# Kernel optimization log

Hardware: AMD Instinct MI355X
Metric: run time of the kernel (lower is better)

The kernel has to match this reference:

```python
import jax, jax.numpy as jnp
import numpy as np

D_MODEL = 768
N_LAYER = 2
VOCAB = 32000
D_STATE = 16
D_INNER = 1536
DT_RANK = 48
D_CONV = 4
B, L = 2, 1024
EPS = 1e-5


def rmsnorm(x, w):
    return x * jax.lax.rsqrt(jnp.mean(x * x, axis=-1, keepdims=True) + EPS) * w


def selective_scan(u, dt, A, Bm, Cm, Dv):
    # u: (b,l,d)  dt: (b,l,d)  A: (d,n)  Bm,Cm: (b,l,n)  Dv: (d,)
    dA = jnp.einsum('bld,dn->bldn', dt, A)
    dB_u = jnp.einsum('bld,bld,bln->bldn', dt, u, Bm)
    # shift dA left by one step along l, zero-pad at end, reverse-cumsum, exp
    t = jnp.concatenate([dA[:, 1:], jnp.zeros_like(dA[:, :1])], axis=1)
    dA_cumsum = jnp.exp(jnp.flip(jnp.cumsum(jnp.flip(t, axis=1), axis=1), axis=1))
    x = dB_u * dA_cumsum
    x = jnp.cumsum(x, axis=1) / (dA_cumsum + 1e-12)
    y = jnp.einsum('bldn,bln->bld', x, Cm)
    return y + u * Dv


def mamba_block(x, W_in, conv_w, conv_b, x_proj_w, dt_proj_w, dt_proj_b, A_log, D_param, W_out):
    b, l, d = x.shape
    xz = x @ W_in.T                       # (b,l,2*d_inner)
    xs, res = xz[..., :D_INNER], xz[..., D_INNER:]
    # depthwise causal conv1d: left-pad d_conv-1 -> output length l
    xt = jnp.transpose(xs, (0, 2, 1))     # (b,d_in,l)
    xt = jax.lax.conv_general_dilated(
        xt, conv_w, window_strides=(1,), padding=[(D_CONV - 1, 0)],
        dimension_numbers=('NCH', 'OIH', 'NCH'), feature_group_count=D_INNER)
    xt = xt + conv_b[None, :, None]
    xs = jax.nn.silu(jnp.transpose(xt, (0, 2, 1)))
    # SSM
    A = -jnp.exp(A_log.astype(jnp.float32))
    x_dbl = xs @ x_proj_w.T               # (b,l,dt_rank+2n)
    delta = x_dbl[..., :DT_RANK]
    Bm = x_dbl[..., DT_RANK:DT_RANK + D_STATE]
    Cm = x_dbl[..., DT_RANK + D_STATE:]
    delta = jax.nn.softplus(delta @ dt_proj_w.T + dt_proj_b)
    y = selective_scan(xs, delta, A, Bm, Cm, D_param.astype(jnp.float32))
    y = y * jax.nn.silu(res)
    return y @ W_out.T


def setup_inputs() -> dict:
    key = jax.random.key(0)
    ks = jax.random.split(key, 12)
    s = 0.02
    inp = {
        'input_ids': jax.random.randint(ks[0], (B, L), 0, VOCAB),
        'embedding': jax.random.normal(ks[1], (VOCAB, D_MODEL), jnp.float32) * s,
        'W_in': jax.random.normal(ks[2], (N_LAYER, 2 * D_INNER, D_MODEL), jnp.float32) * s,
        'conv_w': jax.random.normal(ks[3], (N_LAYER, D_INNER, 1, D_CONV), jnp.float32) * 0.2,
        'conv_b': jnp.zeros((N_LAYER, D_INNER), jnp.float32),
        'x_proj_w': jax.random.normal(ks[4], (N_LAYER, DT_RANK + 2 * D_STATE, D_INNER), jnp.float32) * s,
        'dt_proj_w': jax.random.normal(ks[5], (N_LAYER, D_INNER, DT_RANK), jnp.float32) * s,
        'dt_proj_b': jnp.full((N_LAYER, D_INNER), -4.0, jnp.float32),
        'A_log': jnp.broadcast_to(jnp.log(jnp.arange(1, D_STATE + 1, dtype=jnp.float32)), (N_LAYER, D_INNER, D_STATE)) * jnp.ones((N_LAYER, D_INNER, 1), jnp.float32),
        'D_param': jnp.ones((N_LAYER, D_INNER), jnp.float32),
        'W_out': jax.random.normal(ks[6], (N_LAYER, D_MODEL, D_INNER), jnp.float32) * s,
        'norm_w': jnp.ones((N_LAYER, D_MODEL), jnp.float32),
        'norm_f_w': jnp.ones((D_MODEL,), jnp.float32),
    }
    return inp


def reference(input_ids, embedding, W_in, conv_w, conv_b, x_proj_w, dt_proj_w,
              dt_proj_b, A_log, D_param, W_out, norm_w, norm_f_w):
    x = embedding[input_ids]              # (b,l,d_model)
    for i in range(N_LAYER):
        x = mamba_block(rmsnorm(x, norm_w[i]), W_in[i], conv_w[i], conv_b[i],
                        x_proj_w[i], dt_proj_w[i], dt_proj_b[i], A_log[i],
                        D_param[i], W_out[i]) + x
    x = rmsnorm(x, norm_f_w)
    return x @ embedding.T                # tied lm_head -> (b,l,vocab)
```

## Files before the change

kernel.cpp:

```cpp
#include <hip/hip_runtime.h>
#include <math.h>

#define DM    768
#define DS    16
#define DI    1536
#define DTR   48
#define NB    2
#define NL    1024
#define NBL   (NB*NL)
#define NVOC  32000
#define XDL   128

typedef __attribute__((ext_vector_type(8))) short bf16x8;
typedef __attribute__((ext_vector_type(4))) float floatx4;

static __device__ __forceinline__ float siluf(float x){ return x / (1.0f + expf(-x)); }
static __device__ __forceinline__ float softplusf(float x){ return (x > 20.0f) ? x : log1pf(expf(x)); }
static __device__ __forceinline__ unsigned short f2bf(float f){
    unsigned int u = __float_as_uint(f);
    u += 0x7FFFu + ((u >> 16) & 1u);
    return (unsigned short)(u >> 16);
}

#define GLL16(g, l) __builtin_amdgcn_global_load_lds( \
    (const __attribute__((address_space(1))) unsigned int*)(g), \
    (__attribute__((address_space(3))) unsigned int*)(l), 16, 0, 0)

__global__ __launch_bounds__(256) void cast_bf16_kernel(const float* __restrict__ in,
        unsigned short* __restrict__ out, int n4){
    int i = blockIdx.x*256 + threadIdx.x;
    if (i >= n4) return;
    float4 v = ((const float4*)in)[i];
    ushort4 o = { f2bf(v.x), f2bf(v.y), f2bf(v.z), f2bf(v.w) };
    ((ushort4*)out)[i] = o;
}

__global__ __launch_bounds__(256) void cast_pad_xproj_kernel(const float* __restrict__ in,
        unsigned short* __restrict__ out){
    int q = blockIdx.x*256 + threadIdx.x;
    const int QL = 128*1536/4;
    if (q >= 2*QL) return;
    int layer = q / QL, rem = q - layer*QL;
    int row = rem / (1536/4), c4 = rem - row*(1536/4);
    ushort4 o = {0,0,0,0};
    if (row < 80){
        float4 v = ((const float4*)(in + ((size_t)layer*80 + row)*1536))[c4];
        o.x = f2bf(v.x); o.y = f2bf(v.y); o.z = f2bf(v.z); o.w = f2bf(v.w);
    }
    ((ushort4*)out)[q] = o;
}

__global__ __launch_bounds__(256) void zero_f32_kernel(float* __restrict__ p, int n4){
    int i = blockIdx.x*256 + threadIdx.x;
    if (i >= n4) return;
    float4 z = {0.f,0.f,0.f,0.f};
    ((float4*)p)[i] = z;
}

__global__ __launch_bounds__(256) void embed_kernel(const int* __restrict__ ids,
        const float* __restrict__ emb, float* __restrict__ x){
    int i = blockIdx.x*256 + threadIdx.x;
    if (i >= NBL*DM) return;
    int row = i / DM, c = i - row*DM;
    x[i] = emb[(size_t)ids[row]*DM + c];
}

__global__ __launch_bounds__(256) void rmsnorm_bf16_kernel(const float* __restrict__ x,
        const float* __restrict__ w, unsigned short* __restrict__ h){
    int row = blockIdx.x;
    const float* xr = x + (size_t)row*DM;
    __shared__ float red[256];
    float s = 0.f;
    for (int c = threadIdx.x; c < DM; c += 256){ float v = xr[c]; s += v*v; }
    red[threadIdx.x] = s; __syncthreads();
    for (int o = 128; o > 0; o >>= 1){
        if (threadIdx.x < o) red[threadIdx.x] += red[threadIdx.x + o];
        __syncthreads();
    }
    float r = 1.0f / sqrtf(red[0]*(1.0f/DM) + 1e-5f);
    for (int c = threadIdx.x; c < DM; c += 256) h[(size_t)row*DM + c] = f2bf(xr[c]*r*w[c]);
}

template<int MODE>
__global__ __launch_bounds__(256) void mfma_gemm_nt(const unsigned short* __restrict__ A,
        const unsigned short* __restrict__ B, float* __restrict__ C,
        int M, int N, int K, int Kc){
    __shared__ __align__(16) unsigned short Asm[128*32];
    __shared__ __align__(16) unsigned short Bsm[128*32];
    int tid = threadIdx.x;

    int nwg  = gridDim.x * gridDim.y;
    int orig = blockIdx.y * gridDim.x + blockIdx.x;
    int q = nwg >> 3, r = nwg & 7;
    int xcd = orig & 7;
    int wg  = (xcd < r ? xcd*(q+1) : r*(q+1) + (xcd-r)*q) + (orig >> 3);
    int mb  = wg % gridDim.y;
    int nb  = wg / gridDim.y;
    int m0 = mb * 128, n0 = nb * 128;

    int lane = tid & 63;
    int quad = lane >> 4, l16 = lane & 15;
    int wave = tid >> 6;
    int wm = (wave >> 1) * 64, wn = (wave & 1) * 64;

    floatx4 acc[4][4] = {};

    int srow = tid >> 2, skcol = (tid & 3) * 8;
    const unsigned short* Ag = A + (size_t)(m0 + srow) * K + skcol;
    const unsigned short* Bg = B + (size_t)(n0 + srow) * K + skcol;
    size_t half = (size_t)64 * K;

    int k0 = blockIdx.z * Kc;
    for (int kt = k0; kt < k0 + Kc; kt += 32){
        GLL16(Ag + kt,        &Asm[(size_t)tid*8]);
        GLL16(Ag + kt + half, &Asm[2048 + (size_t)tid*8]);
        GLL16(Bg + kt,        &Bsm[(size_t)tid*8]);
        GLL16(Bg + kt + half, &Bsm[2048 + (size_t)tid*8]);
        __syncthreads();

        bf16x8 af[4], bff[4];
        #pragma unroll
        for (int i = 0; i < 4; i++){
            af[i]  = *(const bf16x8*)&Asm[(wm + i*16 + l16)*32 + quad*8];
            bff[i] = *(const bf16x8*)&Bsm[(wn + i*16 + l16)*32 + quad*8];
        }
        #pragma unroll
        for (int i = 0; i < 4; i++)
            #pragma unroll
            for (int j = 0; j < 4; j++)
                acc[i][j] = __builtin_amdgcn_mfma_f32_16x16x32_bf16(af[i], bff[j], acc[i][j], 0, 0, 0);
        __syncthreads();
    }

    #pragma unroll
    for (int i = 0; i < 4; i++){
        int gm = m0 + wm + i*16 + quad*4;
        #pragma unroll
        for (int j = 0; j < 4; j++){
            int gn = n0 + wn + j*16 + l16;
            float* cp = C + (size_t)gm*N + gn;
            #pragma unroll
            for (int r = 0; r < 4; r++){
                float v = acc[i][j][r];
                if (MODE == 2){
                    atomicAdd(&cp[(size_t)r*N], v);
                } else {
                    if (MODE == 1) v += cp[(size_t)r*N];
                    cp[(size_t)r*N] = v;
                }
            }
        }
    }
}

__global__ __launch_bounds__(256) void gemm_nt(const float* __restrict__ A,
        const float* __restrict__ Bw, float* __restrict__ C, const float* __restrict__ bias,
        int M, int N, int K, int lda, int ldb, int ldc, int act, int accum){
    __shared__ float As[16][68];
    __shared__ float Bs[16][68];
    int tid = threadIdx.x;
    int tn = tid & 15, tm = tid >> 4;
    int n0 = blockIdx.x * 64, m0 = blockIdx.y * 64;
    float acc[4][4] = {{0.f}};
    for (int kt = 0; kt < K; kt += 16){
        int gk = kt + tn;
        bool kok = gk < K;
        #pragma unroll
        for (int r = 0; r < 4; r++){
            int m = tm + r*16;
            As[tn][m] = (kok && (m0 + m) < M) ? A[(size_t)(m0+m)*lda + gk] : 0.f;
            Bs[tn][m] = (kok && (n0 + m) < N) ? Bw[(size_t)(n0+m)*ldb + gk] : 0.f;
        }
        __syncthreads();
        #pragma unroll
        for (int kk = 0; kk < 16; kk++){
            float a0 = As[kk][tm*4+0], a1 = As[kk][tm*4+1], a2 = As[kk][tm*4+2], a3 = As[kk][tm*4+3];
            float b0 = Bs[kk][tn*4+0], b1 = Bs[kk][tn*4+1], b2 = Bs[kk][tn*4+2], b3 = Bs[kk][tn*4+3];
            acc[0][0] += a0*b0; acc[0][1] += a0*b1; acc[0][2] += a0*b2; acc[0][3] += a0*b3;
            acc[1][0] += a1*b0; acc[1][1] += a1*b1; acc[1][2] += a1*b2; acc[1][3] += a1*b3;
            acc[2][0] += a2*b0; acc[2][1] += a2*b1; acc[2][2] += a2*b2; acc[2][3] += a2*b3;
            acc[3][0] += a3*b0; acc[3][1] += a3*b1; acc[3][2] += a3*b2; acc[3][3] += a3*b3;
        }
        __syncthreads();
    }
    #pragma unroll
    for (int i = 0; i < 4; i++){
        int gm = m0 + tm*4 + i;
        if (gm >= M) continue;
        #pragma unroll
        for (int j = 0; j < 4; j++){
            int gn = n0 + tn*4 + j;
            if (gn >= N) continue;
            float v = acc[i][j];
            if (bias) v += bias[gn];
            if (act == 1) v = softplusf(v);
            size_t ci = (size_t)gm*ldc + gn;
            if (accum) v += C[ci];
            C[ci] = v;
        }
    }
}

__global__ __launch_bounds__(256) void conv_silu_kernel(const float* __restrict__ xz,
        const float* __restrict__ cw, const float* __restrict__ cb,
        float* __restrict__ xs, unsigned short* __restrict__ xs_bf){
    int i = blockIdx.x*256 + threadIdx.x;
    if (i >= NBL*DI) return;
    int bl = i / DI, d = i - bl*DI;
    int l = bl & (NL-1);
    float acc = cb[d];
    #pragma unroll
    for (int j = 0; j < 4; j++){
        int off = j - 3;
        if (l + off >= 0) acc += cw[d*4+j] * xz[(size_t)(bl + off)*(2*DI) + d];
    }
    float v = siluf(acc);
    xs[i] = v;
    xs_bf[i] = f2bf(v);
}

__global__ __launch_bounds__(256) void transpose_kernel(const float* __restrict__ in,
        float* __restrict__ out, int R, int Ccols, int ldin){
    __shared__ float tile[32][33];
    int c0 = blockIdx.x*32, r0 = blockIdx.y*32;
    int tx = threadIdx.x & 31, ty = threadIdx.x >> 5;
    #pragma unroll
    for (int i = 0; i < 32; i += 8){
        int r = r0 + ty + i, c = c0 + tx;
        tile[ty+i][tx] = (r < R && c < Ccols) ? in[(size_t)r*ldin + c] : 0.f;
    }
    __syncthreads();
    #pragma unroll
    for (int i = 0; i < 32; i += 8){
        int r = r0 + tx, c = c0 + ty + i;
        if (c < Ccols && r < R) out[(size_t)c*R + r] = tile[tx][ty+i];
    }
}

static __device__ __forceinline__ float block_scan_excl(float v, float* sbuf, float* total){
    int tid  = threadIdx.x;
    int lane = tid & 63, w = tid >> 6;
    float run = v;
    #pragma unroll
    for (int s = 1; s < 64; s <<= 1){
        float t = __shfl_up(run, s, 64);
        if (lane >= s) run += t;
    }
    if (lane == 63) sbuf[w] = run;
    __syncthreads();
    float w0 = sbuf[0], w1 = sbuf[1], w2 = sbuf[2], w3 = sbuf[3];
    __syncthreads();
    float wpre = 0.f;
    if (w > 0) wpre += w0;
    if (w > 1) wpre += w1;
    if (w > 2) wpre += w2;
    *total = w0 + w1 + w2 + w3;
    return wpre + run - v;
}

__global__ __launch_bounds__(256) void scan_kernel(const float* __restrict__ u_t,
        const float* dt_t, const float* __restrict__ xdbl_t,
        const float* __restrict__ A_log, const float* __restrict__ Dp,
        float* y_t){
    __shared__ float sbuf[8];
    int tid = threadIdx.x;
    int bd = blockIdx.x;
    int b = bd / DI, d = bd - b*DI;
    size_t rowoff = (size_t)d*NBL + b*NL;
    int l0 = tid*4;

    float4 dtv = *(const float4*)(dt_t + rowoff + l0);
    float4 uv  = *(const float4*)(u_t  + rowoff + l0);
    float d4[4] = {dtv.x, dtv.y, dtv.z, dtv.w};
    float u4[4] = {uv.x,  uv.y,  uv.z,  uv.w};
    float pl[4], du[4], yac[4] = {0.f,0.f,0.f,0.f};
    float run = 0.f;
    #pragma unroll
    for (int r = 0; r < 4; r++){ run += d4[r]; pl[r] = run; du[r] = d4[r]*u4[r]; }
    float T;
    float ex = block_scan_excl(run, sbuf, &T);
    #pragma unroll
    for (int r = 0; r < 4; r++) pl[r] += ex;

    for (int n = 0; n < DS; n++){
        float An = -expf(A_log[d*DS + n]);
        float4 Bv4 = *(const float4*)(xdbl_t + (size_t)(DTR+n)*NBL + b*NL + l0);
        float4 Cv4 = *(const float4*)(xdbl_t + (size_t)(DTR+DS+n)*NBL + b*NL + l0);
        float Bv[4] = {Bv4.x, Bv4.y, Bv4.z, Bv4.w};
        float Cv[4] = {Cv4.x, Cv4.y, Cv4.z, Cv4.w};
        float e[4], zl[4];
        float zrun = 0.f;
        #pragma unroll
        for (int r = 0; r < 4; r++){
            e[r] = expf(An * (T - pl[r]));
            zrun += du[r]*Bv[r]*e[r];
            zl[r] = zrun;
        }
        float zt;
        float zex = block_scan_excl(zrun, sbuf, &zt);
        #pragma unroll
        for (int r = 0; r < 4; r++){
            float num = zex + zl[r];
            float xv  = num / (e[r] + 1e-12f);
            yac[r] += xv * Cv[r];
        }
    }
    float Dv = Dp[d];
    float4 yo;
    yo.x = yac[0] + u4[0]*Dv;
    yo.y = yac[1] + u4[1]*Dv;
    yo.z = yac[2] + u4[2]*Dv;
    yo.w = yac[3] + u4[3]*Dv;
    *(float4*)(y_t + rowoff + l0) = yo;
}

__global__ __launch_bounds__(256) void gate_transpose_kernel(const float* __restrict__ y_t,
        const float* __restrict__ xz, unsigned short* __restrict__ ys){
    __shared__ float tile[32][33];
    int c0 = blockIdx.x*32;
    int r0 = blockIdx.y*32;
    int tx = threadIdx.x & 31, ty = threadIdx.x >> 5;
    #pragma unroll
    for (int i = 0; i < 32; i += 8)
        tile[ty+i][tx] = y_t[(size_t)(r0+ty+i)*NBL + (c0+tx)];
    __syncthreads();
    #pragma unroll
    for (int i = 0; i < 32; i += 8){
        int d  = r0 + tx;
        int bl = c0 + ty + i;
        float g = siluf(xz[(size_t)bl*(2*DI) + DI + d]);
        ys[(size_t)bl*DI + d] = f2bf(tile[tx][ty+i] * g);
    }
}

extern "C" void kernel_launch(void* const* d_in, const int* in_sizes, int n_in,
                              void* d_out, int out_size, void* d_ws, size_t ws_size,
                              hipStream_t stream){
    const int*   ids    = (const int*)d_in[0];
    const float* emb    = (const float*)d_in[1];
    const float* W_in   = (const float*)d_in[2];
    const float* convw  = (const float*)d_in[3];
    const float* convb  = (const float*)d_in[4];
    const float* xproj  = (const float*)d_in[5];
    const float* dtw    = (const float*)d_in[6];
    const float* dtbias = (const float*)d_in[7];
    const float* Alog   = (const float*)d_in[8];
    const float* Dpar   = (const float*)d_in[9];
    const float* Wout   = (const float*)d_in[10];
    const float* normw  = (const float*)d_in[11];
    const float* normf  = (const float*)d_in[12];
    float* out = (float*)d_out;

    float* ws    = (float*)d_ws;
    float* x     = ws;
    float* xz    = x     + (size_t)NBL*DM;
    float* xs    = xz    + (size_t)NBL*2*DI;
    float* xdbl  = xs    + (size_t)NBL*DI;
    float* xdblt = xdbl  + (size_t)NBL*XDL;
    float* dtb   = xdblt + (size_t)NBL*80;
    float* dtt   = dtb   + (size_t)NBL*DI;
    float* ut    = dtt   + (size_t)NBL*DI;
    unsigned short* h_bf   = (unsigned short*)(ut + (size_t)NBL*DI);
    unsigned short* emb_bf = h_bf    + (size_t)NBL*DM;
    unsigned short* win_bf = emb_bf  + (size_t)NVOC*DM;
    unsigned short* wout_bf= win_bf  + (size_t)2*2*DI*DM;
    unsigned short* xs_bf  = wout_bf + (size_t)2*DM*DI;
    unsigned short* xprojp = xs_bf   + (size_t)NBL*DI;
    unsigned short* ys_bf  = (unsigned short*)dtb;
    float* yt = dtt;

    cast_bf16_kernel<<<(NVOC*DM/4 + 255)/256, 256, 0, stream>>>(emb, emb_bf, NVOC*DM/4);
    cast_bf16_kernel<<<(2*2*DI*DM/4 + 255)/256, 256, 0, stream>>>(W_in, win_bf, 2*2*DI*DM/4);
    cast_bf16_kernel<<<(2*DM*DI/4 + 255)/256, 256, 0, stream>>>(Wout, wout_bf, 2*DM*DI/4);
    cast_pad_xproj_kernel<<<(2*128*1536/4 + 255)/256, 256, 0, stream>>>(xproj, xprojp);

    embed_kernel<<<(NBL*DM + 255)/256, 256, 0, stream>>>(ids, emb, x);

    for (int i = 0; i < 2; i++){
        rmsnorm_bf16_kernel<<<NBL, 256, 0, stream>>>(x, normw + i*DM, h_bf);
        mfma_gemm_nt<0><<<dim3(3072/128, NBL/128, 1), 256, 0, stream>>>(
                h_bf, win_bf + (size_t)i*2*DI*DM, xz, NBL, 2*DI, DM, DM);
        conv_silu_kernel<<<(NBL*DI + 255)/256, 256, 0, stream>>>(xz, convw + i*DI*4, convb + i*DI, xs, xs_bf);
        zero_f32_kernel<<<(NBL*XDL/4 + 255)/256, 256, 0, stream>>>(xdbl, NBL*XDL/4);
        mfma_gemm_nt<2><<<dim3(1, NBL/128, 8), 256, 0, stream>>>(
                xs_bf, xprojp + (size_t)i*128*DI, xdbl, NBL, XDL, DI, DI/8);
        gemm_nt<<<dim3(24,32), 256, 0, stream>>>(xdbl, dtw + (size_t)i*DI*DTR, dtb, dtbias + i*DI,
                NBL, DI, DTR, XDL, DTR, DI, 1, 0);
        transpose_kernel<<<dim3(3,64),  256, 0, stream>>>(xdbl, xdblt, NBL, 80, XDL);
        transpose_kernel<<<dim3(48,64), 256, 0, stream>>>(dtb,  dtt,   NBL, DI, DI);
        transpose_kernel<<<dim3(48,64), 256, 0, stream>>>(xs,   ut,    NBL, DI, DI);
        scan_kernel<<<NB*DI, 256, 0, stream>>>(ut, dtt, xdblt,
                Alog + (size_t)i*DI*DS, Dpar + i*DI, yt);
        gate_transpose_kernel<<<dim3(64,48), 256, 0, stream>>>(yt, xz, ys_bf);
        mfma_gemm_nt<2><<<dim3(DM/128, NBL/128, 2), 256, 0, stream>>>(
                ys_bf, wout_bf + (size_t)i*DM*DI, x, NBL, DM, DI, DI/2);
    }

    rmsnorm_bf16_kernel<<<NBL, 256, 0, stream>>>(x, normf, h_bf);
    mfma_gemm_nt<0><<<dim3(NVOC/128, NBL/128, 1), 256, 0, stream>>>(
            h_bf, emb_bf, out, NBL, NVOC, DM, DM);
}
```

Baseline: 898.3 us.

## Deepen GEMM K-tile with swizzled LDS, wave-level scan, fuse transposes

The MFMA GEMM now stages a 64-wide K tile per iteration and XOR-swizzles the LDS layout, which halves the barrier count per K and aims to reduce bank conflicts. The selective scan assigns one wavefront per (batch, channel) row with 16 elements per lane, replacing block-level scans and their LDS barriers with pure shuffle scans. The two dt/u transposes are merged into one kernel launch. The trade-offs are double the LDS per GEMM block and higher register pressure in the scan.

```diff
diff --git a/kernel.cpp b/kernel.cpp
--- a/kernel.cpp
+++ b/kernel.cpp
@@ -85,8 +85,8 @@
 __global__ __launch_bounds__(256) void mfma_gemm_nt(const unsigned short* __restrict__ A,
         const unsigned short* __restrict__ B, float* __restrict__ C,
         int M, int N, int K, int Kc){
-    __shared__ __align__(16) unsigned short Asm[128*32];
-    __shared__ __align__(16) unsigned short Bsm[128*32];
+    __shared__ __align__(16) unsigned short Asm[128*64];
+    __shared__ __align__(16) unsigned short Bsm[128*64];
     int tid = threadIdx.x;
 
     int nwg  = gridDim.x * gridDim.y;
@@ -105,30 +105,36 @@
 
     floatx4 acc[4][4] = {};
 
-    int srow = tid >> 2, skcol = (tid & 3) * 8;
-    const unsigned short* Ag = A + (size_t)(m0 + srow) * K + skcol;
-    const unsigned short* Bg = B + (size_t)(n0 + srow) * K + skcol;
-    size_t half = (size_t)64 * K;
+    int srow = tid >> 3;
+    int csrc = ((tid & 7) ^ ((tid >> 3) & 7)) * 8;
+    const unsigned short* Ag = A + (size_t)(m0 + srow) * K + csrc;
+    const unsigned short* Bg = B + (size_t)(n0 + srow) * K + csrc;
 
     int k0 = blockIdx.z * Kc;
-    for (int kt = k0; kt < k0 + Kc; kt += 32){
-        GLL16(Ag + kt,        &Asm[(size_t)tid*8]);
-        GLL16(Ag + kt + half, &Asm[2048 + (size_t)tid*8]);
-        GLL16(Bg + kt,        &Bsm[(size_t)tid*8]);
-        GLL16(Bg + kt + half, &Bsm[2048 + (size_t)tid*8]);
+    for (int kt = k0; kt < k0 + Kc; kt += 64){
+        #pragma unroll
+        for (int qr = 0; qr < 4; qr++){
+            GLL16(Ag + (size_t)qr*32*K + kt, &Asm[((size_t)qr*256 + tid)*8]);
+            GLL16(Bg + (size_t)qr*32*K + kt, &Bsm[((size_t)qr*256 + tid)*8]);
+        }
         __syncthreads();
 
-        bf16x8 af[4], bff[4];
-        #pragma unroll
-        for (int i = 0; i < 4; i++){
-            af[i]  = *(const bf16x8*)&Asm[(wm + i*16 + l16)*32 + quad*8];
-            bff[i] = *(const bf16x8*)&Bsm[(wn + i*16 + l16)*32 + quad*8];
-        }
-        #pragma unroll
-        for (int i = 0; i < 4; i++)
+        #pragma unroll
+        for (int ks = 0; ks < 2; ks++){
+            bf16x8 af[4], bff[4];
             #pragma unroll
-            for (int j = 0; j < 4; j++)
-                acc[i][j] = __builtin_amdgcn_mfma_f32_16x16x32_bf16(af[i], bff[j], acc[i][j], 0, 0, 0);
+            for (int i = 0; i < 4; i++){
+                int ar = wm + i*16 + l16;
+                af[i]  = *(const bf16x8*)&Asm[ar*64 + ((ks*4 + quad) ^ (ar & 7))*8];
+                int br = wn + i*16 + l16;
+                bff[i] = *(const bf16x8*)&Bsm[br*64 + ((ks*4 + quad) ^ (br & 7))*8];
+            }
+            #pragma unroll
+            for (int i = 0; i < 4; i++)
+                #pragma unroll
+                for (int j = 0; j < 4; j++)
+                    acc[i][j] = __builtin_amdgcn_mfma_f32_16x16x32_bf16(af[i], bff[j], acc[i][j], 0, 0, 0);
+        }
         __syncthreads();
     }
 
@@ -140,13 +146,13 @@
             int gn = n0 + wn + j*16 + l16;
             float* cp = C + (size_t)gm*N + gn;
             #pragma unroll
-            for (int r = 0; r < 4; r++){
-                float v = acc[i][j][r];
+            for (int rr = 0; rr < 4; rr++){
+                float v = acc[i][j][rr];
                 if (MODE == 2){
-                    atomicAdd(&cp[(size_t)r*N], v);
+                    atomicAdd(&cp[(size_t)rr*N], v);
                 } else {
-                    if (MODE == 1) v += cp[(size_t)r*N];
-                    cp[(size_t)r*N] = v;
+                    if (MODE == 1) v += cp[(size_t)rr*N];
+                    cp[(size_t)rr*N] = v;
                 }
             }
         }
@@ -237,81 +243,101 @@
     }
 }
 
-static __device__ __forceinline__ float block_scan_excl(float v, float* sbuf, float* total){
-    int tid  = threadIdx.x;
-    int lane = tid & 63, w = tid >> 6;
-    float run = v;
+__global__ __launch_bounds__(256) void transpose2_kernel(const float* __restrict__ in1,
+        float* __restrict__ out1, const float* __restrict__ in2, float* __restrict__ out2){
+    __shared__ float tile[32][33];
+    int c0 = blockIdx.x*32, r0 = blockIdx.y*32;
+    int tx = threadIdx.x & 31, ty = threadIdx.x >> 5;
+    #pragma unroll
+    for (int i = 0; i < 32; i += 8)
+        tile[ty+i][tx] = in1[(size_t)(r0+ty+i)*DI + (c0+tx)];
+    __syncthreads();
+    #pragma unroll
+    for (int i = 0; i < 32; i += 8)
+        out1[(size_t)(c0+ty+i)*NBL + (r0+tx)] = tile[tx][ty+i];
+    __syncthreads();
+    #pragma unroll
+    for (int i = 0; i < 32; i += 8)
+        tile[ty+i][tx] = in2[(size_t)(r0+ty+i)*DI + (c0+tx)];
+    __syncthreads();
+    #pragma unroll
+    for (int i = 0; i < 32; i += 8)
+        out2[(size_t)(c0+ty+i)*NBL + (r0+tx)] = tile[tx][ty+i];
+}
+
+static __device__ __forceinline__ float wave_incl_scan(float v, int lane){
     #pragma unroll
     for (int s = 1; s < 64; s <<= 1){
-        float t = __shfl_up(run, s, 64);
-        if (lane >= s) run += t;
-    }
-    if (lane == 63) sbuf[w] = run;
-    __syncthreads();
-    float w0 = sbuf[0], w1 = sbuf[1], w2 = sbuf[2], w3 = sbuf[3];
-    __syncthreads();
-    float wpre = 0.f;
-    if (w > 0) wpre += w0;
-    if (w > 1) wpre += w1;
-    if (w > 2) wpre += w2;
-    *total = w0 + w1 + w2 + w3;
-    return wpre + run - v;
+        float t = __shfl_up(v, s, 64);
+        if (lane >= s) v += t;
+    }
+    return v;
 }
 
 __global__ __launch_bounds__(256) void scan_kernel(const float* __restrict__ u_t,
         const float* dt_t, const float* __restrict__ xdbl_t,
         const float* __restrict__ A_log, const float* __restrict__ Dp,
         float* y_t){
-    __shared__ float sbuf[8];
-    int tid = threadIdx.x;
-    int bd = blockIdx.x;
+    int tid = threadIdx.x, lane = tid & 63, w = tid >> 6;
+    int bd = blockIdx.x*4 + w;
     int b = bd / DI, d = bd - b*DI;
     size_t rowoff = (size_t)d*NBL + b*NL;
-    int l0 = tid*4;
-
-    float4 dtv = *(const float4*)(dt_t + rowoff + l0);
-    float4 uv  = *(const float4*)(u_t  + rowoff + l0);
-    float d4[4] = {dtv.x, dtv.y, dtv.z, dtv.w};
-    float u4[4] = {uv.x,  uv.y,  uv.z,  uv.w};
-    float pl[4], du[4], yac[4] = {0.f,0.f,0.f,0.f};
+    int l0 = lane*16;
+
+    float d16[16], u16[16];
+    #pragma unroll
+    for (int q = 0; q < 4; q++){
+        float4 v = ((const float4*)(dt_t + rowoff + l0))[q];
+        d16[q*4+0]=v.x; d16[q*4+1]=v.y; d16[q*4+2]=v.z; d16[q*4+3]=v.w;
+        float4 u = ((const float4*)(u_t + rowoff + l0))[q];
+        u16[q*4+0]=u.x; u16[q*4+1]=u.y; u16[q*4+2]=u.z; u16[q*4+3]=u.w;
+    }
+    float pl[16], yac[16];
     float run = 0.f;
     #pragma unroll
-    for (int r = 0; r < 4; r++){ run += d4[r]; pl[r] = run; du[r] = d4[r]*u4[r]; }
-    float T;
-    float ex = block_scan_excl(run, sbuf, &T);
-    #pragma unroll
-    for (int r = 0; r < 4; r++) pl[r] += ex;
+    for (int r = 0; r < 16; r++){ run += d16[r]; pl[r] = run; yac[r] = 0.f; }
+    float inc = wave_incl_scan(run, lane);
+    float ex  = inc - run;
+    float T   = __shfl(inc, 63, 64);
+    #pragma unroll
+    for (int r = 0; r < 16; r++) pl[r] += ex;
 
     for (int n = 0; n < DS; n++){
         float An = -expf(A_log[d*DS + n]);
-        float4 Bv4 = *(const float4*)(xdbl_t + (size_t)(DTR+n)*NBL + b*NL + l0);
-        float4 Cv4 = *(const float4*)(xdbl_t + (size_t)(DTR+DS+n)*NBL + b*NL + l0);
-        float Bv[4] = {Bv4.x, Bv4.y, Bv4.z, Bv4.w};
-        float Cv[4] = {Cv4.x, Cv4.y, Cv4.z, Cv4.w};
-        float e[4], zl[4];
+        float Bv[16], Cv[16];
+        #pragma unroll
+        for (int q = 0; q < 4; q++){
+            float4 bv = ((const float4*)(xdbl_t + (size_t)(DTR+n)*NBL + b*NL + l0))[q];
+            Bv[q*4+0]=bv.x; Bv[q*4+1]=bv.y; Bv[q*4+2]=bv.z; Bv[q*4+3]=bv.w;
+            float4 cv = ((const float4*)(xdbl_t + (size_t)(DTR+DS+n)*NBL + b*NL + l0))[q];
+            Cv[q*4+0]=cv.x; Cv[q*4+1]=cv.y; Cv[q*4+2]=cv.z; Cv[q*4+3]=cv.w;
+        }
+        float e[16], zl[16];
         float zrun = 0.f;
         #pragma unroll
-        for (int r = 0; r < 4; r++){
+        for (int r = 0; r < 16; r++){
             e[r] = expf(An * (T - pl[r]));
-            zrun += du[r]*Bv[r]*e[r];
+            zrun += d16[r]*u16[r]*Bv[r]*e[r];
             zl[r] = zrun;
         }
-        float zt;
-        float zex = block_scan_excl(zrun, sbuf, &zt);
-        #pragma unroll
-        for (int r = 0; r < 4; r++){
+        float zinc = wave_incl_scan(zrun, lane);
+        float zex  = zinc - zrun;
+        #pragma unroll
+        for (int r = 0; r < 16; r++){
             float num = zex + zl[r];
-            float xv  = num / (e[r] + 1e-12f);
-            yac[r] += xv * Cv[r];
+            yac[r] += num / (e[r] + 1e-12f) * Cv[r];
         }
     }
     float Dv = Dp[d];
-    float4 yo;
-    yo.x = yac[0] + u4[0]*Dv;
-    yo.y = yac[1] + u4[1]*Dv;
-    yo.z = yac[2] + u4[2]*Dv;
-    yo.w = yac[3] + u4[3]*Dv;
-    *(float4*)(y_t + rowoff + l0) = yo;
+    #pragma unroll
+    for (int q = 0; q < 4; q++){
+        float4 yo;
+        yo.x = yac[q*4+0] + u16[q*4+0]*Dv;
+        yo.y = yac[q*4+1] + u16[q*4+1]*Dv;
+        yo.z = yac[q*4+2] + u16[q*4+2]*Dv;
+        yo.w = yac[q*4+3] + u16[q*4+3]*Dv;
+        ((float4*)(y_t + rowoff + l0))[q] = yo;
+    }
 }
 
 __global__ __launch_bounds__(256) void gate_transpose_kernel(const float* __restrict__ y_t,
@@ -387,9 +413,8 @@
         gemm_nt<<<dim3(24,32), 256, 0, stream>>>(xdbl, dtw + (size_t)i*DI*DTR, dtb, dtbias + i*DI,
                 NBL, DI, DTR, XDL, DTR, DI, 1, 0);
         transpose_kernel<<<dim3(3,64),  256, 0, stream>>>(xdbl, xdblt, NBL, 80, XDL);
-        transpose_kernel<<<dim3(48,64), 256, 0, stream>>>(dtb,  dtt,   NBL, DI, DI);
-        transpose_kernel<<<dim3(48,64), 256, 0, stream>>>(xs,   ut,    NBL, DI, DI);
-        scan_kernel<<<NB*DI, 256, 0, stream>>>(ut, dtt, xdblt,
+        transpose2_kernel<<<dim3(48,64), 256, 0, stream>>>(dtb, dtt, xs, ut);
+        scan_kernel<<<NB*DI/4, 256, 0, stream>>>(ut, dtt, xdblt,
                 Alog + (size_t)i*DI*DS, Dpar + i*DI, yt);
         gate_transpose_kernel<<<dim3(64,48), 256, 0, stream>>>(yt, xz, ys_bf);
         mfma_gemm_nt<2><<<dim3(DM/128, NBL/128, 2), 256, 0, stream>>>(
```

New measurement: 888.8 us. About the same (-1.1%).
